# Performance work log

Hardware: AMD Instinct MI355X
Metric: run time of the kernel (lower is better)

The kernel has to match this reference:

```python
import jax, jax.numpy as jnp
import numpy as np

N_MOLS = 2048
DEPTH = 4

def _graph_conv(fatoms, fbonds, agraph, bgraph, Wi, Wh, Wo, bo):
    # fbonds: [n_bonds, 88] -> nei_input_h: [n_bonds, H]
    nei_input_h = fbonds @ Wi.T
    msg = jax.nn.relu(nei_input_h)
    for _ in range(DEPTH - 1):
        # gather neighbor bond messages [n_bonds, max_nei, H], sum over neighbors
        nei = msg[bgraph].sum(axis=1)
        msg = jax.nn.relu(nei_input_h + nei @ Wh.T)
    # aggregate bond messages into atoms: [n_atoms, max_nei, H] -> [n_atoms, H]
    atom_nei = msg[agraph].sum(axis=1)
    atom_in = jnp.concatenate([fatoms, atom_nei], axis=1)  # [n_atoms, 82+H]
    return jax.nn.relu(atom_in @ Wo.T + bo)

def _mol_embed(atom_h, mol_idx):
    return jax.ops.segment_sum(atom_h, mol_idx, num_segments=N_MOLS)

def setup_inputs() -> dict:
    key = jax.random.key(0)
    ks = jax.random.split(key, 24)
    n_atoms, n_bonds, max_nei, H = 100000, 200000, 10, 256
    d = {}
    d['fatoms_src'] = jax.random.normal(ks[0], (n_atoms, 82), jnp.float32)
    d['fbonds_src'] = jax.random.normal(ks[1], (n_bonds, 88), jnp.float32)
    d['agraph_src'] = jax.random.randint(ks[2], (n_atoms, max_nei), 0, n_bonds, jnp.int32)
    d['bgraph_src'] = jax.random.randint(ks[3], (n_bonds, max_nei), 0, n_bonds, jnp.int32)
    d['mol_idx_src'] = jnp.sort(jax.random.randint(ks[4], (n_atoms,), 0, N_MOLS, jnp.int32))
    d['fatoms_tgt'] = jax.random.normal(ks[5], (n_atoms, 82), jnp.float32)
    d['fbonds_tgt'] = jax.random.normal(ks[6], (n_bonds, 88), jnp.float32)
    d['agraph_tgt'] = jax.random.randint(ks[7], (n_atoms, max_nei), 0, n_bonds, jnp.int32)
    d['bgraph_tgt'] = jax.random.randint(ks[8], (n_bonds, max_nei), 0, n_bonds, jnp.int32)
    d['mol_idx_tgt'] = jnp.sort(jax.random.randint(ks[9], (n_atoms,), 0, N_MOLS, jnp.int32))
    s = 0.05
    d['Wi_s'] = jax.random.normal(ks[10], (H, 88), jnp.float32) * s
    d['Wh_s'] = jax.random.normal(ks[11], (H, H), jnp.float32) * s
    d['Wo_s'] = jax.random.normal(ks[12], (H, 82 + H), jnp.float32) * s
    d['bo_s'] = jax.random.normal(ks[13], (H,), jnp.float32) * s
    d['Wi_t'] = jax.random.normal(ks[14], (H, 88), jnp.float32) * s
    d['Wh_t'] = jax.random.normal(ks[15], (H, H), jnp.float32) * s
    d['Wo_t'] = jax.random.normal(ks[16], (H, 82 + H), jnp.float32) * s
    d['bo_t'] = jax.random.normal(ks[17], (H,), jnp.float32) * s
    d['Wrh'] = jax.random.normal(ks[18], (H, H), jnp.float32) * s
    d['brh'] = jax.random.normal(ks[19], (H,), jnp.float32) * s
    d['Wro'] = jax.random.normal(ks[20], (1, H), jnp.float32) * s
    d['bro'] = jax.random.normal(ks[21], (1,), jnp.float32) * s
    return d

def reference(fatoms_src, fbonds_src, agraph_src, bgraph_src, mol_idx_src,
              fatoms_tgt, fbonds_tgt, agraph_tgt, bgraph_tgt, mol_idx_tgt,
              Wi_s, Wh_s, Wo_s, bo_s, Wi_t, Wh_t, Wo_t, bo_t,
              Wrh, brh, Wro, bro):
    src_atom_h = _graph_conv(fatoms_src, fbonds_src, agraph_src, bgraph_src, Wi_s, Wh_s, Wo_s, bo_s)
    src_mol_h = _mol_embed(src_atom_h, mol_idx_src)
    tgt_atom_h = _graph_conv(fatoms_tgt, fbonds_tgt, agraph_tgt, bgraph_tgt, Wi_t, Wh_t, Wo_t, bo_t)
    tgt_mol_h = _mol_embed(tgt_atom_h, mol_idx_tgt)
    rxn_h = jax.nn.relu((tgt_mol_h - src_mol_h) @ Wrh.T + brh)
    return rxn_h @ Wro.T + bro  # [N_MOLS, 1]
```

## Files before the change

kernel.cpp:

```cpp
#include <hip/hip_runtime.h>

typedef _Float16 f16;
using f16x8 = __attribute__((ext_vector_type(8))) _Float16;
using f32x4 = __attribute__((ext_vector_type(4))) float;

#define H 256
#define NM 2048

__device__ __forceinline__ void gload_lds16(const f16* g, f16* lds)
{
    __builtin_amdgcn_global_load_lds(
        (const __attribute__((address_space(1))) void*)g,
        (__attribute__((address_space(3))) void*)lds, 16, 0, 0);
}

__global__ __launch_bounds__(256) void gemm_mfma(
    const float* __restrict__ A1, int lda1, int K1r,
    const f16*  __restrict__ W1, int K1p,
    const f16*  __restrict__ A2, int lda2, int K2,
    const f16*  __restrict__ W2,
    const float* __restrict__ bias, f16* __restrict__ C, int M, int N)
{
    __shared__ f16 As[128][64];
    __shared__ f16 Bs[128][64];

    const int bm = blockIdx.x * 128;
    const int bn = blockIdx.y * 128;
    const int tid  = threadIdx.x;
    const int wave = tid >> 6, lane = tid & 63;
    const int wr = wave >> 1, wc = wave & 1;
    const int lrow = lane & 15;
    const int kg   = lane >> 4;
    const int swz  = lrow & 7;

    const int glr = lane >> 3;
    const int glc = lane & 7;
    const int gsc = glc ^ glr;

    f32x4 acc[4][4];
    #pragma unroll
    for (int m = 0; m < 4; ++m)
        #pragma unroll
        for (int n = 0; n < 4; ++n)
            acc[m][n] = (f32x4){0.f, 0.f, 0.f, 0.f};

    auto mfma_body = [&]() {
        #pragma unroll
        for (int ks = 0; ks < 2; ++ks) {
            f16x8 af[4], bf[4];
            const int cc = ((ks * 4 + kg) ^ swz) * 8;
            #pragma unroll
            for (int m = 0; m < 4; ++m)
                af[m] = *(const f16x8*)&As[wr * 64 + m * 16 + lrow][cc];
            #pragma unroll
            for (int n = 0; n < 4; ++n)
                bf[n] = *(const f16x8*)&Bs[wc * 64 + n * 16 + lrow][cc];
            #pragma unroll
            for (int m = 0; m < 4; ++m)
                #pragma unroll
                for (int n = 0; n < 4; ++n)
                    acc[m][n] = __builtin_amdgcn_mfma_f32_16x16x32_f16(af[m], bf[n], acc[m][n], 0, 0, 0);
        }
    };

    if (A1 != nullptr) {
        for (int k0 = 0; k0 < K1p; k0 += 64) {
            {
                int row = tid >> 1;
                int h0  = (tid & 1) * 32;
                int gr  = bm + row;
                const float* srcp = A1 + (size_t)gr * lda1 + k0 + h0;
                f16 tmp[32];
                #pragma unroll
                for (int i = 0; i < 32; i += 2) {
                    float x = 0.f, y = 0.f;
                    int gk = k0 + h0 + i;
                    if (gr < M) {
                        if (gk + 1 < K1r) { float2 v = *(const float2*)(srcp + i); x = v.x; y = v.y; }
                        else if (gk < K1r) { x = srcp[i]; }
                    }
                    tmp[i] = (f16)x; tmp[i + 1] = (f16)y;
                }
                int rs = row & 7;
                int gb = h0 >> 3;
                #pragma unroll
                for (int j = 0; j < 4; ++j)
                    *(float4*)&As[row][((gb + j) ^ rs) * 8] = *(float4*)&tmp[j * 8];
            }
            #pragma unroll
            for (int q = 0; q < 4; ++q) {
                int row = wave * 32 + q * 8 + glr;
                gload_lds16(W1 + (size_t)(bn + row) * K1p + k0 + gsc * 8,
                            &Bs[wave * 32 + q * 8][0]);
            }
            __syncthreads();
            mfma_body();
            __syncthreads();
        }
    }

    if (A2 != nullptr) {
        for (int k0 = 0; k0 < K2; k0 += 64) {
            #pragma unroll
            for (int q = 0; q < 4; ++q) {
                int row = wave * 32 + q * 8 + glr;
                gload_lds16(A2 + (size_t)(bm + row) * lda2 + k0 + gsc * 8,
                            &As[wave * 32 + q * 8][0]);
                gload_lds16(W2 + (size_t)(bn + row) * K2 + k0 + gsc * 8,
                            &Bs[wave * 32 + q * 8][0]);
            }
            __syncthreads();
            mfma_body();
            __syncthreads();
        }
    }

    #pragma unroll
    for (int m = 0; m < 4; ++m) {
        #pragma unroll
        for (int n = 0; n < 4; ++n) {
            int gc = bn + wc * 64 + n * 16 + lrow;
            float bv = bias ? bias[gc] : 0.f;
            int gr0 = bm + wr * 64 + m * 16 + kg * 4;
            #pragma unroll
            for (int r = 0; r < 4; ++r) {
                int gr = gr0 + r;
                if (gr < M) C[(size_t)gr * N + gc] = (f16)fmaxf(acc[m][n][r] + bv, 0.f);
            }
        }
    }
}

__global__ __launch_bounds__(256) void convert_w(
    const float* __restrict__ src, int lds_, int koff, int kvalid,
    f16* __restrict__ dst, int Kd)
{
    int n = blockIdx.x;
    for (int k = threadIdx.x; k < Kd; k += 256) {
        float v = (k < kvalid) ? src[(size_t)n * lds_ + koff + k] : 0.f;
        dst[(size_t)n * Kd + k] = (f16)v;
    }
}

__global__ __launch_bounds__(256) void gather_sum10(
    const f16* __restrict__ src, const int* __restrict__ idx,
    f16* __restrict__ dst, int n_rows)
{
    int row  = blockIdx.x * 8 + (threadIdx.x >> 5);
    int lane = threadIdx.x & 31;
    if (row >= n_rows) return;
    const int* ip = idx + (size_t)row * 10;
    float s[8] = {};
    #pragma unroll
    for (int j = 0; j < 10; ++j) {
        int r = ip[j];
        float4 v = *((const float4*)(src + (size_t)r * H) + lane);
        const f16* pb = (const f16*)&v;
        #pragma unroll
        for (int e = 0; e < 8; ++e) s[e] += (float)pb[e];
    }
    f16 o[8];
    #pragma unroll
    for (int e = 0; e < 8; ++e) o[e] = (f16)s[e];
    *((float4*)(dst + (size_t)row * H) + lane) = *(const float4*)o;
}

__global__ __launch_bounds__(256) void segsum(
    const f16* __restrict__ atom_h, const int* __restrict__ mol_idx,
    float* __restrict__ mol_h, int n_atoms)
{
    int m = blockIdx.x;
    int lo = 0, hi = n_atoms;
    while (lo < hi) { int mid = (lo + hi) >> 1; if (mol_idx[mid] < m) lo = mid + 1; else hi = mid; }
    int start = lo;
    hi = n_atoms;
    while (lo < hi) { int mid = (lo + hi) >> 1; if (mol_idx[mid] < m + 1) lo = mid + 1; else hi = mid; }
    int end = lo;
    int c = threadIdx.x;
    float s = 0.f;
    for (int a = start; a < end; ++a) s += (float)atom_h[(size_t)a * H + c];
    mol_h[(size_t)m * H + c] = s;
}

__global__ __launch_bounds__(256) void diff_kernel(
    const float* __restrict__ a, const float* __restrict__ b,
    f16* __restrict__ c, int n)
{
    int i = blockIdx.x * 256 + threadIdx.x;
    if (i < n) c[i] = (f16)(a[i] - b[i]);
}

__global__ __launch_bounds__(256) void final_dot(
    const f16* __restrict__ rxn, const float* __restrict__ Wro,
    const float* __restrict__ bro, float* __restrict__ out)
{
    int m = blockIdx.x;
    int t = threadIdx.x;
    float v = (float)rxn[(size_t)m * H + t] * Wro[t];
    #pragma unroll
    for (int off = 32; off; off >>= 1) v += __shfl_down(v, off, 64);
    __shared__ float red[4];
    if ((t & 63) == 0) red[t >> 6] = v;
    __syncthreads();
    if (t == 0) out[m] = red[0] + red[1] + red[2] + red[3] + bro[0];
}

static void run_graph(const float* fatoms, const float* fbonds, const int* agraph,
                      const int* bgraph, const int* mol_idx,
                      const f16* Wi16, const f16* Wh16, const f16* Wo1, const f16* Wo2,
                      const float* fbonds_f32, const float* bo,
                      f16* bufA, f16* bufB, float* molh,
                      int n_atoms, int n_bonds, hipStream_t stream)
{
    dim3 gb((n_bonds + 127) / 128, 2);
    dim3 ga((n_atoms + 127) / 128, 2);

    gemm_mfma<<<gb, 256, 0, stream>>>(fbonds_f32, 88, 88, Wi16, 128,
                                      (const f16*)nullptr, 0, 0, (const f16*)nullptr,
                                      (const float*)nullptr, bufA, n_bonds, H);
    for (int it = 0; it < 3; ++it) {
        gather_sum10<<<(n_bonds + 7) / 8, 256, 0, stream>>>(bufA, bgraph, bufB, n_bonds);
        gemm_mfma<<<gb, 256, 0, stream>>>(fbonds_f32, 88, 88, Wi16, 128,
                                          bufB, H, H, Wh16,
                                          (const float*)nullptr, bufA, n_bonds, H);
    }
    gather_sum10<<<(n_atoms + 7) / 8, 256, 0, stream>>>(bufA, agraph, bufB, n_atoms);
    gemm_mfma<<<ga, 256, 0, stream>>>(fatoms, 82, 82, Wo1, 128,
                                      bufB, H, H, Wo2,
                                      bo, bufA, n_atoms, H);
    segsum<<<NM, 256, 0, stream>>>(bufA, mol_idx, molh, n_atoms);
}

extern "C" void kernel_launch(void* const* d_in, const int* in_sizes, int n_in,
                              void* d_out, int out_size, void* d_ws, size_t ws_size,
                              hipStream_t stream)
{
    const float* fatoms_src = (const float*)d_in[0];
    const float* fbonds_src = (const float*)d_in[1];
    const int*   agraph_src = (const int*)d_in[2];
    const int*   bgraph_src = (const int*)d_in[3];
    const int*   mol_idx_src= (const int*)d_in[4];
    const float* fatoms_tgt = (const float*)d_in[5];
    const float* fbonds_tgt = (const float*)d_in[6];
    const int*   agraph_tgt = (const int*)d_in[7];
    const int*   bgraph_tgt = (const int*)d_in[8];
    const int*   mol_idx_tgt= (const int*)d_in[9];
    const float* Wi_s = (const float*)d_in[10];
    const float* Wh_s = (const float*)d_in[11];
    const float* Wo_s = (const float*)d_in[12];
    const float* bo_s = (const float*)d_in[13];
    const float* Wi_t = (const float*)d_in[14];
    const float* Wh_t = (const float*)d_in[15];
    const float* Wo_t = (const float*)d_in[16];
    const float* bo_t = (const float*)d_in[17];
    const float* Wrh  = (const float*)d_in[18];
    const float* brh  = (const float*)d_in[19];
    const float* Wro  = (const float*)d_in[20];
    const float* bro  = (const float*)d_in[21];

    const int n_atoms = in_sizes[0] / 82;
    const int n_bonds = in_sizes[1] / 88;

    char* ws = (char*)d_ws;
    size_t off = 0;
    auto alloc = [&](size_t bytes) { size_t o = off; off = (off + bytes + 255) & ~(size_t)255; return o; };
    f16*   bufA = (f16*)(ws + alloc((size_t)n_bonds * H * 2));
    f16*   bufB = (f16*)(ws + alloc((size_t)n_bonds * H * 2));
    float* molS = (float*)(ws + alloc((size_t)NM * H * 4));
    float* molT = (float*)(ws + alloc((size_t)NM * H * 4));
    f16*   dbuf = (f16*)(ws + alloc((size_t)NM * H * 2));
    f16*   rxn  = (f16*)(ws + alloc((size_t)NM * H * 2));
    f16* Wi16_s = (f16*)(ws + alloc(256 * 128 * 2));
    f16* Wh16_s = (f16*)(ws + alloc(256 * 256 * 2));
    f16* Wo1_s  = (f16*)(ws + alloc(256 * 128 * 2));
    f16* Wo2_s  = (f16*)(ws + alloc(256 * 256 * 2));
    f16* Wi16_t = (f16*)(ws + alloc(256 * 128 * 2));
    f16* Wh16_t = (f16*)(ws + alloc(256 * 256 * 2));
    f16* Wo1_t  = (f16*)(ws + alloc(256 * 128 * 2));
    f16* Wo2_t  = (f16*)(ws + alloc(256 * 256 * 2));
    f16* Wrh16  = (f16*)(ws + alloc(256 * 256 * 2));

    convert_w<<<256, 256, 0, stream>>>(Wi_s,  88,  0,  88, Wi16_s, 128);
    convert_w<<<256, 256, 0, stream>>>(Wh_s, 256,  0, 256, Wh16_s, 256);
    convert_w<<<256, 256, 0, stream>>>(Wo_s, 338,  0,  82, Wo1_s, 128);
    convert_w<<<256, 256, 0, stream>>>(Wo_s, 338, 82, 256, Wo2_s, 256);
    convert_w<<<256, 256, 0, stream>>>(Wi_t,  88,  0,  88, Wi16_t, 128);
    convert_w<<<256, 256, 0, stream>>>(Wh_t, 256,  0, 256, Wh16_t, 256);
    convert_w<<<256, 256, 0, stream>>>(Wo_t, 338,  0,  82, Wo1_t, 128);
    convert_w<<<256, 256, 0, stream>>>(Wo_t, 338, 82, 256, Wo2_t, 256);
    convert_w<<<256, 256, 0, stream>>>(Wrh, 256,  0, 256, Wrh16, 256);

    run_graph(fatoms_src, fbonds_src, agraph_src, bgraph_src, mol_idx_src,
              Wi16_s, Wh16_s, Wo1_s, Wo2_s, fbonds_src, bo_s,
              bufA, bufB, molS, n_atoms, n_bonds, stream);
    run_graph(fatoms_tgt, fbonds_tgt, agraph_tgt, bgraph_tgt, mol_idx_tgt,
              Wi16_t, Wh16_t, Wo1_t, Wo2_t, fbonds_tgt, bo_t,
              bufA, bufB, molT, n_atoms, n_bonds, stream);

    diff_kernel<<<(NM * H + 255) / 256, 256, 0, stream>>>(molT, molS, dbuf, NM * H);
    dim3 gr(NM / 128, 2);
    gemm_mfma<<<gr, 256, 0, stream>>>((const float*)nullptr, 0, 0, (const f16*)nullptr, 0,
                                      dbuf, H, H, Wrh16,
                                      brh, rxn, NM, H);
    final_dot<<<NM, 256, 0, stream>>>(rxn, Wro, bro, (float*)d_out);
}
```

Measured before the change: 2.640 ms.

## Fuse neighbor gather-sum into GEMM A-tile staging with full-N 64-row tiles

Removes the separate gather_sum10 kernel and computes the 10-neighbor sum directly while staging each A tile in LDS inside the GEMM. The tile shape changes to 64 rows by the full 256 output columns, so each gathered row is computed once instead of once per N-block. This avoids writing and re-reading the intermediate neighbor-sum buffer and saves a launch per iteration. In exchange, the gather latency now sits on the GEMM critical path with no overlap, and messages ping-pong between two buffers.

```diff
diff --git a/kernel.cpp b/kernel.cpp
--- a/kernel.cpp
+++ b/kernel.cpp
@@ -14,21 +14,19 @@
         (__attribute__((address_space(3))) void*)lds, 16, 0, 0);
 }
 
-__global__ __launch_bounds__(256) void gemm_mfma(
+__global__ __launch_bounds__(256) void gemm_fused(
     const float* __restrict__ A1, int lda1, int K1r,
     const f16*  __restrict__ W1, int K1p,
-    const f16*  __restrict__ A2, int lda2, int K2,
-    const f16*  __restrict__ W2,
-    const float* __restrict__ bias, f16* __restrict__ C, int M, int N)
-{
-    __shared__ f16 As[128][64];
-    __shared__ f16 Bs[128][64];
-
-    const int bm = blockIdx.x * 128;
-    const int bn = blockIdx.y * 128;
+    const f16*  __restrict__ src2, const int* __restrict__ idx2, int lda2,
+    const f16*  __restrict__ W2, int K2,
+    const float* __restrict__ bias, f16* __restrict__ C, int M)
+{
+    __shared__ f16 As[64][64];
+    __shared__ f16 Bs[256][64];
+
+    const int bm = blockIdx.x * 64;
     const int tid  = threadIdx.x;
     const int wave = tid >> 6, lane = tid & 63;
-    const int wr = wave >> 1, wc = wave & 1;
     const int lrow = lane & 15;
     const int kg   = lane >> 4;
     const int swz  = lrow & 7;
@@ -36,6 +34,10 @@
     const int glr = lane >> 3;
     const int glc = lane & 7;
     const int gsc = glc ^ glr;
+
+    const int arow = tid >> 2;
+    const int aq   = tid & 3;
+    const int ars  = arow & 7;
 
     f32x4 acc[4][4];
     #pragma unroll
@@ -51,10 +53,10 @@
             const int cc = ((ks * 4 + kg) ^ swz) * 8;
             #pragma unroll
             for (int m = 0; m < 4; ++m)
-                af[m] = *(const f16x8*)&As[wr * 64 + m * 16 + lrow][cc];
+                af[m] = *(const f16x8*)&As[m * 16 + lrow][cc];
             #pragma unroll
             for (int n = 0; n < 4; ++n)
-                bf[n] = *(const f16x8*)&Bs[wc * 64 + n * 16 + lrow][cc];
+                bf[n] = *(const f16x8*)&Bs[wave * 64 + n * 16 + lrow][cc];
             #pragma unroll
             for (int m = 0; m < 4; ++m)
                 #pragma unroll
@@ -63,52 +65,86 @@
         }
     };
 
+    auto stageB = [&](const f16* W, int ldw, int k0) {
+        #pragma unroll
+        for (int q = 0; q < 8; ++q)
+            gload_lds16(W + (size_t)(wave * 64 + q * 8 + glr) * ldw + k0 + gsc * 8,
+                        &Bs[wave * 64 + q * 8][0]);
+    };
+
     if (A1 != nullptr) {
         for (int k0 = 0; k0 < K1p; k0 += 64) {
             {
-                int row = tid >> 1;
-                int h0  = (tid & 1) * 32;
-                int gr  = bm + row;
-                const float* srcp = A1 + (size_t)gr * lda1 + k0 + h0;
-                f16 tmp[32];
+                int gr = bm + arow;
+                const float* srcp = A1 + (size_t)gr * lda1 + k0 + aq * 16;
+                f16 tmp[16];
                 #pragma unroll
-                for (int i = 0; i < 32; i += 2) {
+                for (int i = 0; i < 16; i += 2) {
                     float x = 0.f, y = 0.f;
-                    int gk = k0 + h0 + i;
+                    int gk = k0 + aq * 16 + i;
                     if (gr < M) {
                         if (gk + 1 < K1r) { float2 v = *(const float2*)(srcp + i); x = v.x; y = v.y; }
                         else if (gk < K1r) { x = srcp[i]; }
                     }
                     tmp[i] = (f16)x; tmp[i + 1] = (f16)y;
                 }
-                int rs = row & 7;
-                int gb = h0 >> 3;
-                #pragma unroll
-                for (int j = 0; j < 4; ++j)
-                    *(float4*)&As[row][((gb + j) ^ rs) * 8] = *(float4*)&tmp[j * 8];
+                *(float4*)&As[arow][((aq * 2)     ^ ars) * 8] = *(float4*)&tmp[0];
+                *(float4*)&As[arow][((aq * 2 + 1) ^ ars) * 8] = *(float4*)&tmp[8];
             }
-            #pragma unroll
-            for (int q = 0; q < 4; ++q) {
-                int row = wave * 32 + q * 8 + glr;
-                gload_lds16(W1 + (size_t)(bn + row) * K1p + k0 + gsc * 8,
-                            &Bs[wave * 32 + q * 8][0]);
-            }
+            stageB(W1, K1p, k0);
             __syncthreads();
             mfma_body();
             __syncthreads();
         }
     }
 
-    if (A2 != nullptr) {
+    if (src2 != nullptr) {
         for (int k0 = 0; k0 < K2; k0 += 64) {
-            #pragma unroll
-            for (int q = 0; q < 4; ++q) {
-                int row = wave * 32 + q * 8 + glr;
-                gload_lds16(A2 + (size_t)(bm + row) * lda2 + k0 + gsc * 8,
-                            &As[wave * 32 + q * 8][0]);
-                gload_lds16(W2 + (size_t)(bn + row) * K2 + k0 + gsc * 8,
-                            &Bs[wave * 32 + q * 8][0]);
+            if (idx2 != nullptr) {
+                int gr = bm + arow;
+                f16 tmp[16];
+                int ip[10];
+                if (gr < M) {
+                    const int* ipp = idx2 + (size_t)gr * 10;
+                    #pragma unroll
+                    for (int j = 0; j < 10; ++j) ip[j] = ipp[j];
+                    {
+                        float s[8] = {};
+                        #pragma unroll
+                        for (int j = 0; j < 10; ++j) {
+                            float4 v = *(const float4*)(src2 + (size_t)ip[j] * lda2 + k0 + aq * 16);
+                            const f16* pb = (const f16*)&v;
+                            #pragma unroll
+                            for (int e = 0; e < 8; ++e) s[e] += (float)pb[e];
+                        }
+                        #pragma unroll
+                        for (int e = 0; e < 8; ++e) tmp[e] = (f16)s[e];
+                    }
+                    {
+                        float s[8] = {};
+                        #pragma unroll
+                        for (int j = 0; j < 10; ++j) {
+                            float4 v = *(const float4*)(src2 + (size_t)ip[j] * lda2 + k0 + aq * 16 + 8);
+                            const f16* pb = (const f16*)&v;
+                            #pragma unroll
+                            for (int e = 0; e < 8; ++e) s[e] += (float)pb[e];
+                        }
+                        #pragma unroll
+                        for (int e = 0; e < 8; ++e) tmp[8 + e] = (f16)s[e];
+                    }
+                } else {
+                    #pragma unroll
+                    for (int e = 0; e < 16; ++e) tmp[e] = (f16)0.f;
+                }
+                *(float4*)&As[arow][((aq * 2)     ^ ars) * 8] = *(float4*)&tmp[0];
+                *(float4*)&As[arow][((aq * 2 + 1) ^ ars) * 8] = *(float4*)&tmp[8];
+            } else {
+                #pragma unroll
+                for (int q = 0; q < 2; ++q)
+                    gload_lds16(src2 + (size_t)(bm + wave * 16 + q * 8 + glr) * lda2 + k0 + gsc * 8,
+                                &As[wave * 16 + q * 8][0]);
             }
+            stageB(W2, K2, k0);
             __syncthreads();
             mfma_body();
             __syncthreads();
@@ -116,16 +152,15 @@
     }
 
     #pragma unroll
-    for (int m = 0; m < 4; ++m) {
+    for (int n = 0; n < 4; ++n) {
+        int gc = wave * 64 + n * 16 + lrow;
+        float bv = bias ? bias[gc] : 0.f;
         #pragma unroll
-        for (int n = 0; n < 4; ++n) {
-            int gc = bn + wc * 64 + n * 16 + lrow;
-            float bv = bias ? bias[gc] : 0.f;
-            int gr0 = bm + wr * 64 + m * 16 + kg * 4;
+        for (int m = 0; m < 4; ++m) {
             #pragma unroll
             for (int r = 0; r < 4; ++r) {
-                int gr = gr0 + r;
-                if (gr < M) C[(size_t)gr * N + gc] = (f16)fmaxf(acc[m][n][r] + bv, 0.f);
+                int gr = bm + m * 16 + kg * 4 + r;
+                if (gr < M) C[(size_t)gr * H + gc] = (f16)fmaxf(acc[m][n][r] + bv, 0.f);
             }
         }
     }
@@ -140,29 +175,6 @@
         float v = (k < kvalid) ? src[(size_t)n * lds_ + koff + k] : 0.f;
         dst[(size_t)n * Kd + k] = (f16)v;
     }
-}
-
-__global__ __launch_bounds__(256) void gather_sum10(
-    const f16* __restrict__ src, const int* __restrict__ idx,
-    f16* __restrict__ dst, int n_rows)
-{
-    int row  = blockIdx.x * 8 + (threadIdx.x >> 5);
-    int lane = threadIdx.x & 31;
-    if (row >= n_rows) return;
-    const int* ip = idx + (size_t)row * 10;
-    float s[8] = {};
-    #pragma unroll
-    for (int j = 0; j < 10; ++j) {
-        int r = ip[j];
-        float4 v = *((const float4*)(src + (size_t)r * H) + lane);
-        const f16* pb = (const f16*)&v;
-        #pragma unroll
-        for (int e = 0; e < 8; ++e) s[e] += (float)pb[e];
-    }
-    f16 o[8];
-    #pragma unroll
-    for (int e = 0; e < 8; ++e) o[e] = (f16)s[e];
-    *((float4*)(dst + (size_t)row * H) + lane) = *(const float4*)o;
 }
 
 __global__ __launch_bounds__(256) void segsum(
@@ -208,27 +220,28 @@
 static void run_graph(const float* fatoms, const float* fbonds, const int* agraph,
                       const int* bgraph, const int* mol_idx,
                       const f16* Wi16, const f16* Wh16, const f16* Wo1, const f16* Wo2,
-                      const float* fbonds_f32, const float* bo,
+                      const float* bo,
                       f16* bufA, f16* bufB, float* molh,
                       int n_atoms, int n_bonds, hipStream_t stream)
 {
-    dim3 gb((n_bonds + 127) / 128, 2);
-    dim3 ga((n_atoms + 127) / 128, 2);
-
-    gemm_mfma<<<gb, 256, 0, stream>>>(fbonds_f32, 88, 88, Wi16, 128,
-                                      (const f16*)nullptr, 0, 0, (const f16*)nullptr,
-                                      (const float*)nullptr, bufA, n_bonds, H);
+    dim3 gb((n_bonds + 63) / 64);
+    dim3 ga((n_atoms + 63) / 64);
+
+    gemm_fused<<<gb, 256, 0, stream>>>(fbonds, 88, 88, Wi16, 128,
+                                       (const f16*)nullptr, (const int*)nullptr, 0,
+                                       (const f16*)nullptr, 0,
+                                       (const float*)nullptr, bufA, n_bonds);
+    f16* cur = bufA; f16* nxt = bufB;
     for (int it = 0; it < 3; ++it) {
-        gather_sum10<<<(n_bonds + 7) / 8, 256, 0, stream>>>(bufA, bgraph, bufB, n_bonds);
-        gemm_mfma<<<gb, 256, 0, stream>>>(fbonds_f32, 88, 88, Wi16, 128,
-                                          bufB, H, H, Wh16,
-                                          (const float*)nullptr, bufA, n_bonds, H);
-    }
-    gather_sum10<<<(n_atoms + 7) / 8, 256, 0, stream>>>(bufA, agraph, bufB, n_atoms);
-    gemm_mfma<<<ga, 256, 0, stream>>>(fatoms, 82, 82, Wo1, 128,
-                                      bufB, H, H, Wo2,
-                                      bo, bufA, n_atoms, H);
-    segsum<<<NM, 256, 0, stream>>>(bufA, mol_idx, molh, n_atoms);
+        gemm_fused<<<gb, 256, 0, stream>>>(fbonds, 88, 88, Wi16, 128,
+                                           cur, bgraph, H, Wh16, H,
+                                           (const float*)nullptr, nxt, n_bonds);
+        f16* t = cur; cur = nxt; nxt = t;
+    }
+    gemm_fused<<<ga, 256, 0, stream>>>(fatoms, 82, 82, Wo1, 128,
+                                       cur, agraph, H, Wo2, H,
+                                       bo, nxt, n_atoms);
+    segsum<<<NM, 256, 0, stream>>>(nxt, mol_idx, molh, n_atoms);
 }
 
 extern "C" void kernel_launch(void* const* d_in, const int* in_sizes, int n_in,
@@ -291,16 +304,15 @@
     convert_w<<<256, 256, 0, stream>>>(Wrh, 256,  0, 256, Wrh16, 256);
 
     run_graph(fatoms_src, fbonds_src, agraph_src, bgraph_src, mol_idx_src,
-              Wi16_s, Wh16_s, Wo1_s, Wo2_s, fbonds_src, bo_s,
+              Wi16_s, Wh16_s, Wo1_s, Wo2_s, bo_s,
               bufA, bufB, molS, n_atoms, n_bonds, stream);
     run_graph(fatoms_tgt, fbonds_tgt, agraph_tgt, bgraph_tgt, mol_idx_tgt,
-              Wi16_t, Wh16_t, Wo1_t, Wo2_t, fbonds_tgt, bo_t,
+              Wi16_t, Wh16_t, Wo1_t, Wo2_t, bo_t,
               bufA, bufB, molT, n_atoms, n_bonds, stream);
 
     diff_kernel<<<(NM * H + 255) / 256, 256, 0, stream>>>(molT, molS, dbuf, NM * H);
-    dim3 gr(NM / 128, 2);
-    gemm_mfma<<<gr, 256, 0, stream>>>((const float*)nullptr, 0, 0, (const f16*)nullptr, 0,
-                                      dbuf, H, H, Wrh16,
-                                      brh, rxn, NM, H);
+    gemm_fused<<<NM / 64, 256, 0, stream>>>((const float*)nullptr, 0, 0, (const f16*)nullptr, 0,
+                                            dbuf, (const int*)nullptr, H, Wrh16, H,
+                                            brh, rxn, NM);
     final_dot<<<NM, 256, 0, stream>>>(rxn, Wro, bro, (float*)d_out);
 }
```

Result: faster. 2.150 ms (-18.6%).
